# Performance work log

Hardware: AMD Instinct MI355X
Metric: run time of the kernel (lower is better)

The kernel has to match this reference:

```python
import jax, jax.numpy as jnp
import numpy as np


def setup_inputs() -> dict:
    key = jax.random.key(0)
    ks = jax.random.split(key, 9)
    B, T, C = 4, 2048, 2048
    E, I, SI = 8, 1408, 5632
    s = lambda k, shape, fan_in: jax.random.normal(k, shape, jnp.float32) * (fan_in ** -0.5)
    return {
        "x": jax.random.normal(ks[0], (B, T, C), jnp.float32),
        "gate_w": s(ks[1], (C, E), C),                  # router: x @ gate_w -> [N,E]
        "expert_gate_w": s(ks[2], (E, C, I), C),        # stacked gate_proj weights
        "expert_up_w": s(ks[3], (E, C, I), C),          # stacked up_proj weights
        "expert_down_w": s(ks[4], (E, I, C), I),        # stacked down_proj weights
        "shared_gate_w": s(ks[5], (C, SI), C),
        "shared_up_w": s(ks[6], (C, SI), C),
        "shared_down_w": s(ks[7], (SI, C), SI),
        "shared_expert_gate_w": s(ks[8], (C, 1), C),
        "top_k": 4,
    }


def reference(x, gate_w, expert_gate_w, expert_up_w, expert_down_w,
              shared_gate_w, shared_up_w, shared_down_w, shared_expert_gate_w, top_k):
    B, T, C = x.shape
    E = gate_w.shape[1]
    xf = x.reshape(-1, C)                      # [N, C]
    N = xf.shape[0]

    # --- router: softmax (fp32) -> top-k -> renormalize ---
    logits = xf @ gate_w                       # [N, E]
    probs = jax.nn.softmax(logits.astype(jnp.float32), axis=-1)
    w, idx = jax.lax.top_k(probs, top_k)       # [N, k]
    w = w / jnp.sum(w, axis=-1, keepdims=True)

    # dense combine gates [N, E]: zero for non-selected experts (equivalent to
    # the torch dispatch/sort/combine: each token gets weight w_k on expert idx_k)
    gates = jnp.zeros((N, E), jnp.float32).at[jnp.arange(N)[:, None], idx].add(w)

    # --- per-expert SwiGLU MLP, accumulated via scan over experts ---
    def step(acc, ew):
        wg, wu, wd, g = ew                     # wg/wu: [C,I], wd: [I,C], g: [N]
        h = jax.nn.silu(xf @ wg) * (xf @ wu)   # [N, I]
        return acc + g[:, None] * (h @ wd), None

    routed, _ = jax.lax.scan(
        step, jnp.zeros_like(xf),
        (expert_gate_w, expert_up_w, expert_down_w, gates.T))

    # --- shared expert with sigmoid gate ---
    shared = (jax.nn.silu(xf @ shared_gate_w) * (xf @ shared_up_w)) @ shared_down_w
    sg = jax.nn.sigmoid(xf @ shared_expert_gate_w)   # [N, 1]

    return (routed + sg * shared).reshape(B, T, C)
```

## Files before the change

kernel.cpp:

```cpp
#include <hip/hip_runtime.h>
#include <hip/hip_bf16.h>
#include <stdint.h>


typedef float f32x4 __attribute__((ext_vector_type(4)));
typedef int   i32x4 __attribute__((ext_vector_type(4)));
typedef __hip_bfloat16 bf16;

#define DEV __device__ __forceinline__

DEV void mfma16(f32x4& c, const i32x4& a, const i32x4& b) {
    asm("v_mfma_f32_16x16x32_bf16 %0, %1, %2, %0" : "+v"(c) : "v"(a), "v"(b));
}

template<int ROWS>
DEV void stage(const bf16* gtile, long ldK, char* lds, int tid) {
    const int wid = tid >> 6, lane = tid & 63;
    const int swz = ((lane & 7) ^ (lane >> 3)) << 4;
    constexpr int NISS = (ROWS * 128) / 4096;
    #pragma unroll
    for (int i = 0; i < NISS; i++) {
        const int o = i * 4096 + wid * 1024;
        const int row = (o >> 7) + (lane >> 3);
        const char* ga = (const char*)gtile + (long)row * (ldK * 2) + swz;
        __builtin_amdgcn_global_load_lds(
            (const __attribute__((address_space(1))) void*)ga,
            (__attribute__((address_space(3))) void*)(lds + o), 16, 0, 0);
    }
}

template<int ROWS>
DEV void stage_idx(const char* base, const long* roff, int ktb, char* lds,
                   int tid, int swz) {
    const int wid = tid >> 6;
    constexpr int NISS = (ROWS * 128) / 4096;
    #pragma unroll
    for (int i = 0; i < NISS; i++) {
        const int o = i * 4096 + wid * 1024;
        const char* ga = base + roff[i] + ktb + swz;
        __builtin_amdgcn_global_load_lds(
            (const __attribute__((address_space(1))) void*)ga,
            (__attribute__((address_space(3))) void*)(lds + o), 16, 0, 0);
    }
}

DEV i32x4 ldsfrag(const char* lds, int row, int kbyte) {
    const int off = (row << 7) + (kbyte ^ ((row & 7) << 4));
    return *(const i32x4*)(lds + off);
}

DEV void tcore(unsigned short (*t)[72], const float* __restrict__ src,
               bf16* __restrict__ dst, long Cd, long dld, int cb, int rb,
               int tid) {
    const int s = tid & 15, g = tid >> 4;
    #pragma unroll
    for (int i = 0; i < 4; i++) {
        const int r = i * 16 + g;
        const float4 v = *(const float4*)(src + (long)(rb + r) * Cd + cb + 4 * s);
        union { bf16 h[4]; ushort4 u; } cu;
        cu.h[0] = __float2bfloat16(v.x); cu.h[1] = __float2bfloat16(v.y);
        cu.h[2] = __float2bfloat16(v.z); cu.h[3] = __float2bfloat16(v.w);
        *(ushort4*)&t[r][4 * s] = cu.u;
    }
    __syncthreads();
    #pragma unroll
    for (int i = 0; i < 4; i++) {
        const int c = i * 16 + g;
        ushort4 u;
        u.x = t[4 * s + 0][c]; u.y = t[4 * s + 1][c];
        u.z = t[4 * s + 2][c]; u.w = t[4 * s + 3][c];
        *(ushort4*)((unsigned short*)dst + (long)(cb + c) * dld + rb + 4 * s) = u;
    }
}

__global__ __launch_bounds__(256) void convt_gu(const float* __restrict__ egw,
        const float* __restrict__ euw, const float* __restrict__ sgw,
        const float* __restrict__ suw, bf16* __restrict__ Wea,
        bf16* __restrict__ Web, bf16* __restrict__ Wsa, bf16* __restrict__ Wsb) {
    __shared__ unsigned short t[64][72];
    const int z = blockIdx.z, cb = blockIdx.x * 64, rb = blockIdx.y * 64;
    const float* src; bf16* dst; long Cd;
    if (z < 8)       { src = egw + (long)z * 2048 * 1408;        dst = Wea + (long)z * 1408 * 2048;        Cd = 1408; }
    else if (z < 16) { src = euw + (long)(z - 8) * 2048 * 1408;  dst = Web + (long)(z - 8) * 1408 * 2048;  Cd = 1408; }
    else if (z < 20) { src = sgw + (long)(z - 16) * 1408;        dst = Wsa + (long)(z - 16) * 1408 * 2048; Cd = 5632; }
    else             { src = suw + (long)(z - 20) * 1408;        dst = Wsb + (long)(z - 20) * 1408 * 2048; Cd = 5632; }
    tcore(t, src, dst, Cd, 2048, cb, rb, threadIdx.x);
}

__global__ __launch_bounds__(256) void convt_dns(const float* __restrict__ sdw,
        bf16* __restrict__ Wsd) {
    __shared__ unsigned short t[64][72];
    const int z = blockIdx.z, cb = blockIdx.x * 64, rb = blockIdx.y * 64;
    tcore(t, sdw + (long)z * 1408 * 2048, Wsd + (long)z * 1408,
          2048, 5632, cb, rb, threadIdx.x);
}

__global__ __launch_bounds__(256) void convt_dne(const float* __restrict__ edw,
        bf16* __restrict__ Wed) {
    __shared__ unsigned short t[64][72];
    const int z = blockIdx.z, cb = blockIdx.x * 64, rb = blockIdx.y * 64;
    tcore(t, edw + (long)z * 1408 * 2048, Wed + (long)z * 2048 * 1408,
          2048, 1408, cb, rb, threadIdx.x);
}

__global__ __launch_bounds__(256) void tcvt(const float* __restrict__ srcA,
        bf16* __restrict__ dstA, const float* __restrict__ srcB,
        bf16* __restrict__ dstB, int Cd, long dld, long sz, long dz,
        int zsplit) {
    __shared__ float t[64][65];
    long z = blockIdx.z;
    const float* src; bf16* dst;
    if ((int)z < zsplit) { src = srcA; dst = dstA; }
    else { src = srcB; dst = dstB; z -= zsplit; }
    src += z * sz; dst += z * dz;
    const int cb = blockIdx.x * 64, rb = blockIdx.y * 64;
    const int tx = threadIdx.x & 63, ty = threadIdx.x >> 6;
    #pragma unroll
    for (int i = 0; i < 16; i++) {
        const int r = ty + i * 4;
        t[r][tx] = src[(long)(rb + r) * Cd + cb + tx];
    }
    __syncthreads();
    #pragma unroll
    for (int i = 0; i < 16; i++) {
        const int c = ty + i * 4;
        dst[(long)(cb + c) * dld + rb + tx] = __float2bfloat16(t[tx][c]);
    }
}

__global__ __launch_bounds__(256) void cvtrt(const float* __restrict__ x,
        const float* __restrict__ gw, const float* __restrict__ segw,
        bf16* __restrict__ xb, int* __restrict__ tidx, float* __restrict__ tw,
        float* __restrict__ sg) {
    const int lane = threadIdx.x & 63;
    const long t = (long)blockIdx.x * 4 + (threadIdx.x >> 6);
    const float4* xr = (const float4*)(x + t * 2048);
    ushort4* xo = (ushort4*)(xb + t * 2048);
    float a[9];
    #pragma unroll
    for (int e = 0; e < 9; e++) a[e] = 0.f;
    #pragma unroll
    for (int i = 0; i < 8; i++) {
        const int c4 = i * 64 + lane;
        const float4 v = xr[c4];
        union { bf16 h[4]; ushort4 u; } cu;
        cu.h[0] = __float2bfloat16(v.x); cu.h[1] = __float2bfloat16(v.y);
        cu.h[2] = __float2bfloat16(v.z); cu.h[3] = __float2bfloat16(v.w);
        xo[c4] = cu.u;
        const int c = c4 * 4;
        const float xv[4] = { v.x, v.y, v.z, v.w };
        #pragma unroll
        for (int j = 0; j < 4; j++) {
            const float4* g4 = (const float4*)(gw + (long)(c + j) * 8);
            const float4 g0 = g4[0], g1 = g4[1];
            a[0] += xv[j] * g0.x; a[1] += xv[j] * g0.y;
            a[2] += xv[j] * g0.z; a[3] += xv[j] * g0.w;
            a[4] += xv[j] * g1.x; a[5] += xv[j] * g1.y;
            a[6] += xv[j] * g1.z; a[7] += xv[j] * g1.w;
            a[8] += xv[j] * segw[c + j];
        }
    }
    #pragma unroll
    for (int e = 0; e < 9; e++) {
        #pragma unroll
        for (int o = 32; o; o >>= 1) a[e] += __shfl_xor(a[e], o, 64);
    }
    if (lane == 0) {
        float m = a[0];
        #pragma unroll
        for (int e = 1; e < 8; e++) m = fmaxf(m, a[e]);
        float p[8]; float s = 0.f;
        #pragma unroll
        for (int e = 0; e < 8; e++) { p[e] = expf(a[e] - m); s += p[e]; }
        #pragma unroll
        for (int e = 0; e < 8; e++) p[e] /= s;
        bool used[8] = {false,false,false,false,false,false,false,false};
        float wsum = 0.f; int idx[4]; float wv[4];
        for (int k = 0; k < 4; k++) {
            float best = -1.f; int bi = 0;
            for (int e = 0; e < 8; e++)
                if (!used[e] && p[e] > best) { best = p[e]; bi = e; }
            used[bi] = true; idx[k] = bi; wv[k] = best; wsum += best;
        }
        int4 iv; float4 wv4;
        iv.x = idx[0]; iv.y = idx[1]; iv.z = idx[2]; iv.w = idx[3];
        wv4.x = wv[0] / wsum; wv4.y = wv[1] / wsum;
        wv4.z = wv[2] / wsum; wv4.w = wv[3] / wsum;
        ((int4*)tidx)[t] = iv;
        ((float4*)tw)[t] = wv4;
        sg[t] = 1.f / (1.f + expf(-a[8]));
    }
}

__global__ __launch_bounds__(256) void build_lists(const int* __restrict__ tidx,
        const float* __restrict__ tw, int* __restrict__ tok,
        float* __restrict__ wl, int* __restrict__ cnt, int* __restrict__ inv,
        int N) {
    const int e = blockIdx.x;
    const int tid = threadIdx.x;
    const int per = N / 256;
    __shared__ int csum[256];
    int c = 0;
    for (int i = 0; i < per; i++) {
        const int4 id4 = ((const int4*)tidx)[tid * per + i];
        if (id4.x == e || id4.y == e || id4.z == e || id4.w == e) c++;
    }
    csum[tid] = c;
    __syncthreads();
    for (int o = 1; o < 256; o <<= 1) {
        const int v = (tid >= o) ? csum[tid - o] : 0;
        __syncthreads();
        csum[tid] += v;
        __syncthreads();
    }
    int pos = csum[tid] - c;
    if (tid == 255) cnt[e] = csum[255];
    for (int i = 0; i < per; i++) {
        const int t = tid * per + i;
        const int4   id4 = ((const int4*)tidx)[t];
        const float4 w4  = ((const float4*)tw)[t];
        float w = 0.f; int hit = 0; int k = 0;
        if      (id4.x == e) { w = w4.x; hit = 1; k = 0; }
        else if (id4.y == e) { w = w4.y; hit = 1; k = 1; }
        else if (id4.z == e) { w = w4.z; hit = 1; k = 2; }
        else if (id4.w == e) { w = w4.w; hit = 1; k = 3; }
        if (hit) {
            tok[(long)e * N + pos] = t;
            wl[(long)e * N + pos] = w;
            inv[t * 4 + k] = pos;
            pos++;
        }
    }
}

__global__ void scan8(const int* __restrict__ cnt, int* __restrict__ starts) {
    if (threadIdx.x == 0) {
        int s = 0;
        for (int e = 0; e < 8; e++) { starts[e] = s; s += cnt[e]; }
        starts[8] = s;
    }
}

__global__ __launch_bounds__(256) void megadual(const bf16* __restrict__ A0,
        const int* __restrict__ tok, const int* __restrict__ cnt,
        const int* __restrict__ starts, int nExpZ, int e0,
        const bf16* __restrict__ Wea, const bf16* __restrict__ Web, long ebz,
        const bf16* __restrict__ Wsa, const bf16* __restrict__ Wsb,
        bf16* __restrict__ He, bf16* __restrict__ Hs,
        const float* __restrict__ wl, const float* __restrict__ sg, int K) {
    __shared__ __align__(128) char Al[16384];
    __shared__ __align__(128) char Gl[8192];
    __shared__ __align__(128) char Ul[8192];
    const int z = blockIdx.z;
    const bf16 *BG, *BU; bf16* H; long hld, n0; const float* sc;
    const int* ridx; int Me;
    if (z < nExpZ) {
        const int e = e0 + z;
        Me = cnt[e];
        ridx = tok + (long)e * 8192;
        BG = Wea + (long)z * ebz; BU = Web + (long)z * ebz;
        H = He + ((long)starts[e] - starts[e0]) * 1408;
        hld = 1408; sc = wl + (long)e * 8192;
        n0 = (long)blockIdx.y * 64;
    } else {
        Me = 8192; ridx = nullptr;
        BG = Wsa; BU = Wsb; H = Hs; hld = 5632; sc = sg;
        n0 = (long)((z - nExpZ) * gridDim.y + blockIdx.y) * 64;
    }
    const long m0 = (long)blockIdx.x * 128;
    if (m0 >= Me) return;
    const int tid = threadIdx.x, lane = tid & 63, wid = tid >> 6;
    const int wm = (wid >> 1) * 64, wn = (wid & 1) * 32;
    const int l15 = lane & 15, lhi = lane >> 4;
    const int swz = ((lane & 7) ^ (lane >> 3)) << 4;
    long roffA[4];
    #pragma unroll
    for (int i = 0; i < 4; i++) {
        const int rit = ((i * 4096 + wid * 1024) >> 7) + (lane >> 3);
        int g = (int)m0 + rit;
        if (ridx) g = ridx[g < Me ? g : Me - 1];
        roffA[i] = (long)g * (K * 2);
    }
    f32x4 ag[4][2] = {}; f32x4 au[4][2] = {};
    for (int kt = 0; kt < K; kt += 64) {
        stage_idx<128>((const char*)A0, roffA, kt * 2, Al, tid, swz);
        stage<64>(BG + n0 * K + kt, (long)K, Gl, tid);
        stage<64>(BU + n0 * K + kt, (long)K, Ul, tid);
        __syncthreads();
        #pragma unroll
        for (int ks = 0; ks < 2; ks++) {
            const int kb = ks * 64 + lhi * 16;
            i32x4 af[4], bg[2], bu[2];
            #pragma unroll
            for (int mi = 0; mi < 4; mi++) af[mi] = ldsfrag(Al, wm + mi * 16 + l15, kb);
            #pragma unroll
            for (int ni = 0; ni < 2; ni++) {
                bg[ni] = ldsfrag(Gl, wn + ni * 16 + l15, kb);
                bu[ni] = ldsfrag(Ul, wn + ni * 16 + l15, kb);
            }
            #pragma unroll
            for (int mi = 0; mi < 4; mi++) {
                #pragma unroll
                for (int ni = 0; ni < 2; ni++) {
                    mfma16(ag[mi][ni], af[mi], bg[ni]);
                    mfma16(au[mi][ni], af[mi], bu[ni]);
                }
            }
        }
        __syncthreads();
    }
    asm volatile("s_nop 7\n\ts_nop 7\n\ts_nop 7");
    #pragma unroll
    for (int mi = 0; mi < 4; mi++) {
        #pragma unroll
        for (int r = 0; r < 4; r++) {
            const int pos = (int)m0 + wm + mi * 16 + lhi * 4 + r;
            if (pos < Me) {
                const float s = sc[pos];
                #pragma unroll
                for (int ni = 0; ni < 2; ni++) {
                    const float gv = ag[mi][ni][r], uv = au[mi][ni][r];
                    const float h = (gv / (1.f + expf(-gv))) * uv * s;
                    H[(long)pos * hld + n0 + wn + ni * 16 + l15] = __float2bfloat16(h);
                }
            }
        }
    }
}

template<int TAG>
__global__ __launch_bounds__(256) void gemm_down_t(const bf16* __restrict__ A,
        const bf16* __restrict__ BT, float* __restrict__ C,
        const int* __restrict__ ridx, const int* __restrict__ cntp, int Mfix,
        const int* __restrict__ starts, int ia, int ib,
        int K, long ldc, int beta) {
    __shared__ __align__(128) char Al[16384];
    __shared__ __align__(128) char Bl[16384];
    const int Me = cntp ? *cntp : Mfix;
    const long m0 = (long)blockIdx.y * 128;
    if (m0 >= Me) return;
    if (starts) A += ((long)starts[ia] - starts[ib]) * K;
    const int tid = threadIdx.x, lane = tid & 63, wid = tid >> 6;
    const long n0 = (long)blockIdx.x * 128;
    const int wm = (wid >> 1) * 64, wn = (wid & 1) * 64;
    const int l15 = lane & 15, lhi = lane >> 4;
    f32x4 acc[4][4] = {};
    for (int kt = 0; kt < K; kt += 64) {
        stage<128>(A  + m0 * K + kt, (long)K, Al, tid);
        stage<128>(BT + n0 * K + kt, (long)K, Bl, tid);
        __syncthreads();
        #pragma unroll
        for (int ks = 0; ks < 2; ks++) {
            const int kb = ks * 64 + lhi * 16;
            i32x4 af[4], bfr[4];
            #pragma unroll
            for (int mi = 0; mi < 4; mi++) af[mi]  = ldsfrag(Al, wm + mi * 16 + l15, kb);
            #pragma unroll
            for (int ni = 0; ni < 4; ni++) bfr[ni] = ldsfrag(Bl, wn + ni * 16 + l15, kb);
            #pragma unroll
            for (int mi = 0; mi < 4; mi++) {
                #pragma unroll
                for (int ni = 0; ni < 4; ni++) mfma16(acc[mi][ni], af[mi], bfr[ni]);
            }
        }
        __syncthreads();
    }
    asm volatile("s_nop 7\n\ts_nop 7\n\ts_nop 7");
    #pragma unroll
    for (int mi = 0; mi < 4; mi++) {
        #pragma unroll
        for (int r = 0; r < 4; r++) {
            const int pos = (int)m0 + wm + mi * 16 + lhi * 4 + r;
            if (pos < Me) {
                const long orow = ridx ? (long)ridx[pos] : (long)pos;
                #pragma unroll
                for (int ni = 0; ni < 4; ni++) {
                    const long ci = orow * ldc + n0 + wn + ni * 16 + l15;
                    float v = acc[mi][ni][r];
                    if (beta) v += C[ci];
                    C[ci] = v;
                }
            }
        }
    }
}

__global__ __launch_bounds__(256) void megadown(const bf16* __restrict__ He,
        const bf16* __restrict__ Wd0, long wz, bf16* __restrict__ De,
        const int* __restrict__ cnt, const int* __restrict__ starts, int K) {
    __shared__ __align__(128) char Al[16384];
    __shared__ __align__(128) char Bl[16384];
    const int z = blockIdx.z;
    const int Me = cnt[z];
    const long m0 = (long)blockIdx.y * 128;
    if (m0 >= Me) return;
    const bf16* A  = He + (long)starts[z] * K;
    const bf16* BT = Wd0 + (long)z * wz;
    const int tid = threadIdx.x, lane = tid & 63, wid = tid >> 6;
    const long n0 = (long)blockIdx.x * 128;
    const int wm = (wid >> 1) * 64, wn = (wid & 1) * 64;
    const int l15 = lane & 15, lhi = lane >> 4;
    f32x4 acc[4][4] = {};
    for (int kt = 0; kt < K; kt += 64) {
        stage<128>(A  + m0 * K + kt, (long)K, Al, tid);
        stage<128>(BT + n0 * K + kt, (long)K, Bl, tid);
        __syncthreads();
        #pragma unroll
        for (int ks = 0; ks < 2; ks++) {
            const int kb = ks * 64 + lhi * 16;
            i32x4 af[4], bfr[4];
            #pragma unroll
            for (int mi = 0; mi < 4; mi++) af[mi]  = ldsfrag(Al, wm + mi * 16 + l15, kb);
            #pragma unroll
            for (int ni = 0; ni < 4; ni++) bfr[ni] = ldsfrag(Bl, wn + ni * 16 + l15, kb);
            #pragma unroll
            for (int mi = 0; mi < 4; mi++) {
                #pragma unroll
                for (int ni = 0; ni < 4; ni++) mfma16(acc[mi][ni], af[mi], bfr[ni]);
            }
        }
        __syncthreads();
    }
    asm volatile("s_nop 7\n\ts_nop 7\n\ts_nop 7");
    #pragma unroll
    for (int mi = 0; mi < 4; mi++) {
        #pragma unroll
        for (int r = 0; r < 4; r++) {
            const int pos = (int)m0 + wm + mi * 16 + lhi * 4 + r;
            if (pos < Me) {
                const long orow = (long)starts[z] + pos;
                #pragma unroll
                for (int ni = 0; ni < 4; ni++) {
                    De[orow * 2048 + n0 + wn + ni * 16 + l15]
                        = __float2bfloat16(acc[mi][ni][r]);
                }
            }
        }
    }
}

__global__ __launch_bounds__(256) void reduce4(const bf16* __restrict__ De,
        const int* __restrict__ tidx, const int* __restrict__ inv,
        const int* __restrict__ starts, float* __restrict__ out) {
    const long t = blockIdx.x;
    const int c = threadIdx.x * 8;
    const int4 e4 = ((const int4*)tidx)[t];
    const int4 p4 = ((const int4*)inv)[t];
    long r[4];
    r[0] = (long)starts[e4.x] + p4.x; r[1] = (long)starts[e4.y] + p4.y;
    r[2] = (long)starts[e4.z] + p4.z; r[3] = (long)starts[e4.w] + p4.w;
    float4* o = (float4*)(out + t * 2048 + c);
    float4 o0 = o[0], o1 = o[1];
    float acc[8] = { o0.x, o0.y, o0.z, o0.w, o1.x, o1.y, o1.z, o1.w };
    #pragma unroll
    for (int k = 0; k < 4; k++) {
        const uint4 v = *(const uint4*)(De + r[k] * 2048 + c);
        const unsigned w[4] = { v.x, v.y, v.z, v.w };
        #pragma unroll
        for (int j = 0; j < 4; j++) {
            union { unsigned u; float f; } lo, hi;
            lo.u = (w[j] & 0xffffu) << 16;
            hi.u = w[j] & 0xffff0000u;
            acc[j * 2]     += lo.f;
            acc[j * 2 + 1] += hi.f;
        }
    }
    o[0] = make_float4(acc[0], acc[1], acc[2], acc[3]);
    o[1] = make_float4(acc[4], acc[5], acc[6], acc[7]);
}

extern "C" void kernel_launch(void* const* d_in, const int* in_sizes, int n_in,
                              void* d_out, int out_size, void* d_ws, size_t ws_size,
                              hipStream_t stream) {
    const int N = 8192, Cdim = 2048, E = 8, I = 1408, SI = 5632;

    const float* x    = (const float*)d_in[0];
    const float* gw   = (const float*)d_in[1];
    const float* egw  = (const float*)d_in[2];
    const float* euw  = (const float*)d_in[3];
    const float* edw  = (const float*)d_in[4];
    const float* sgw  = (const float*)d_in[5];
    const float* suw  = (const float*)d_in[6];
    const float* sdw  = (const float*)d_in[7];
    const float* segw = (const float*)d_in[8];
    float* out = (float*)d_out;

    char* ws = (char*)d_ws;
    size_t off = 0;
    auto alloc = [&](size_t bytes) { char* p = ws + off; off += (bytes + 255) & ~(size_t)255; return p; };

    bf16*  xb     = (bf16*) alloc((size_t)N * Cdim * 2);
    int*   tidx   = (int*)  alloc((size_t)N * 4 * 4);
    float* tw     = (float*)alloc((size_t)N * 4 * 4);
    float* sg     = (float*)alloc((size_t)N * 4);
    int*   tok    = (int*)  alloc((size_t)E * N * 4);
    float* wl     = (float*)alloc((size_t)E * N * 4);
    int*   inv    = (int*)  alloc((size_t)N * 4 * 4);
    int*   cnt    = (int*)  alloc(256);
    int*   starts = (int*)  alloc(256);
    const size_t commonEnd = off;

    const size_t EWSLOT = (size_t)E * I * Cdim * 2;
    const size_t SWSLOT = (size_t)SI * Cdim * 2;
    const size_t HROWS  = (size_t)4 * N;
    const size_t mergedNeed = commonEnd + 2 * EWSLOT + 2 * SWSLOT
                            + (size_t)N * SI * 2 + HROWS * I * 2 + 4096;

    cvtrt<<<N / 4, 256, 0, stream>>>(x, gw, segw, xb, tidx, tw, sg);
    build_lists<<<E, 256, 0, stream>>>(tidx, tw, tok, wl, cnt, inv, N);
    scan8<<<1, 64, 0, stream>>>(cnt, starts);

    if (ws_size >= mergedNeed) {
        char* wreg = (char*)alloc(2 * EWSLOT + 2 * SWSLOT);
        bf16* Wea = (bf16*)wreg;
        bf16* Web = (bf16*)(wreg + EWSLOT);
        bf16* Wsa = (bf16*)(wreg + 2 * EWSLOT);
        bf16* Wsb = (bf16*)(wreg + 2 * EWSLOT + SWSLOT);
        bf16* Hs  = (bf16*)alloc((size_t)N * SI * 2);
        bf16* He  = (bf16*)alloc(HROWS * I * 2);
        bf16* Wsd = xb;
        bf16* Wed = Hs;
        bf16* De  = (bf16*)wreg;

        convt_gu<<<dim3(22, 32, 24), 256, 0, stream>>>(
                egw, euw, sgw, suw, Wea, Web, Wsa, Wsb);

        megadual<<<dim3(N / 128, I / 64, E + 4), 256, 0, stream>>>(xb,
                tok, cnt, starts, E, 0, Wea, Web, (long)I * Cdim,
                Wsa, Wsb, He, Hs, wl, sg, Cdim);

        convt_dns<<<dim3(32, 22, 4), 256, 0, stream>>>(sdw, Wsd);
        gemm_down_t<0><<<dim3(Cdim / 128, N / 128), 256, 0, stream>>>(
                Hs, Wsd, out, nullptr, nullptr, N, nullptr, 0, 0,
                SI, (long)Cdim, 0);

        convt_dne<<<dim3(32, 22, 8), 256, 0, stream>>>(edw, Wed);
        megadown<<<dim3(Cdim / 128, N / 128, E), 256, 0, stream>>>(
                He, Wed, (long)Cdim * I, De, cnt, starts, I);
        reduce4<<<N, 256, 0, stream>>>(De, tidx, inv, starts, out);
        return;
    }

    bf16* Wa = (bf16*)alloc(SWSLOT);
    bf16* Wb = (bf16*)alloc(SWSLOT);
    bf16* Wc = (bf16*)alloc(SWSLOT);
    bf16* Hs = (bf16*)alloc((size_t)N * SI * 2);
    bf16* He = (bf16*)alloc(HROWS * I * 2);
    if (off > ws_size) return;

    tcvt<<<dim3(SI / 64, Cdim / 64, 2), 256, 0, stream>>>(
            sgw, Wa, suw, Wb, SI, (long)Cdim, 0, 0, 1);
    tcvt<<<dim3(Cdim / 64, SI / 64, 1), 256, 0, stream>>>(
            sdw, Wc, nullptr, nullptr, Cdim, (long)SI, 0, 0, 1);
    megadual<<<dim3(N / 128, I / 64, 4), 256, 0, stream>>>(xb,
            tok, cnt, starts, 0, 0, nullptr, nullptr, 0,
            Wa, Wb, nullptr, Hs, wl, sg, Cdim);
    gemm_down_t<0><<<dim3(Cdim / 128, N / 128), 256, 0, stream>>>(
            Hs, Wc, out, nullptr, nullptr, N, nullptr, 0, 0, SI, (long)Cdim, 0);

    for (int b = 0; b < 2; b++) {
        const int e0 = b * 4;
        tcvt<<<dim3(I / 64, Cdim / 64, 8), 256, 0, stream>>>(
                egw + (long)e0 * Cdim * I, Wa, euw + (long)e0 * Cdim * I, Wb,
                I, (long)Cdim, (long)Cdim * I, (long)I * Cdim, 4);
        megadual<<<dim3(N / 128, I / 64, 4), 256, 0, stream>>>(xb,
                tok, cnt, starts, 4, e0, Wa, Wb, (long)I * Cdim,
                nullptr, nullptr, He, nullptr, wl, sg, Cdim);
        tcvt<<<dim3(Cdim / 64, I / 64, 4), 256, 0, stream>>>(
                edw + (long)e0 * I * Cdim, Wc, nullptr, nullptr,
                Cdim, (long)I, (long)I * Cdim, (long)Cdim * I, 4);
        for (int z = 0; z < 4; z++) {
            gemm_down_t<1><<<dim3(Cdim / 128, N / 128), 256, 0, stream>>>(
                    He, Wc + (long)z * Cdim * I, out,
                    tok + (long)(e0 + z) * N, cnt + e0 + z, 0,
                    starts, e0 + z, e0, I, (long)Cdim, 1);
        }
    }
}
```

Measured before the change: 1.393 ms.

## Fuse shared down-proj GEMM with routed combine, merge down-weight conversions

When the workspace has room for one more expert weight slot, the two down-projection weight conversions become a single launch. The routed expert down GEMM then runs first, and a new kernel computes the shared down GEMM and adds the four gathered routed expert rows in its epilogue. This removes the separate reduce4 pass and the extra read-modify-write of the fp32 output. The cost is extra workspace, and the epilogue's gather of bf16 De rows is scattered and may not coalesce well. The downfuse epilogue no longer applies the sigmoid shared gate, so it relies on that gate already being folded into Hs.

```diff
diff --git a/kernel.cpp b/kernel.cpp
--- a/kernel.cpp
+++ b/kernel.cpp
@@ -87,6 +87,19 @@
     tcore(t, src, dst, Cd, 2048, cb, rb, threadIdx.x);
 }
 
+__global__ __launch_bounds__(256) void convt_dn(const float* __restrict__ sdw,
+        const float* __restrict__ edw, bf16* __restrict__ Wsd,
+        bf16* __restrict__ Wed) {
+    __shared__ unsigned short t[64][72];
+    const int z = blockIdx.z, cb = blockIdx.x * 64, rb = blockIdx.y * 64;
+    if (z < 4)
+        tcore(t, sdw + (long)z * 1408 * 2048, Wsd + (long)z * 1408,
+              2048, 5632, cb, rb, threadIdx.x);
+    else
+        tcore(t, edw + (long)(z - 4) * 1408 * 2048, Wed + (long)(z - 4) * 2048 * 1408,
+              2048, 1408, cb, rb, threadIdx.x);
+}
+
 __global__ __launch_bounds__(256) void convt_dns(const float* __restrict__ sdw,
         bf16* __restrict__ Wsd) {
     __shared__ unsigned short t[64][72];
@@ -94,7 +107,6 @@
     tcore(t, sdw + (long)z * 1408 * 2048, Wsd + (long)z * 1408,
           2048, 5632, cb, rb, threadIdx.x);
 }
-
 __global__ __launch_bounds__(256) void convt_dne(const float* __restrict__ edw,
         bf16* __restrict__ Wed) {
     __shared__ unsigned short t[64][72];
@@ -385,6 +397,64 @@
     }
 }
 
+__global__ __launch_bounds__(256) void downfuse(const bf16* __restrict__ Hs,
+        const bf16* __restrict__ Wsd, const bf16* __restrict__ De,
+        const int* __restrict__ tidx, const int* __restrict__ inv,
+        const int* __restrict__ starts, float* __restrict__ out, int K) {
+    __shared__ __align__(128) char Al[16384];
+    __shared__ __align__(128) char Bl[16384];
+    __shared__ int sst[8];
+    const int tid = threadIdx.x, lane = tid & 63, wid = tid >> 6;
+    if (tid < 8) sst[tid] = starts[tid];
+    const long m0 = (long)blockIdx.y * 128;
+    const long n0 = (long)blockIdx.x * 128;
+    const int wm = (wid >> 1) * 64, wn = (wid & 1) * 64;
+    const int l15 = lane & 15, lhi = lane >> 4;
+    f32x4 acc[4][4] = {};
+    for (int kt = 0; kt < K; kt += 64) {
+        stage<128>(Hs + m0 * K + kt, (long)K, Al, tid);
+        stage<128>(Wsd + n0 * K + kt, (long)K, Bl, tid);
+        __syncthreads();
+        #pragma unroll
+        for (int ks = 0; ks < 2; ks++) {
+            const int kb = ks * 64 + lhi * 16;
+            i32x4 af[4], bfr[4];
+            #pragma unroll
+            for (int mi = 0; mi < 4; mi++) af[mi]  = ldsfrag(Al, wm + mi * 16 + l15, kb);
+            #pragma unroll
+            for (int ni = 0; ni < 4; ni++) bfr[ni] = ldsfrag(Bl, wn + ni * 16 + l15, kb);
+            #pragma unroll
+            for (int mi = 0; mi < 4; mi++) {
+                #pragma unroll
+                for (int ni = 0; ni < 4; ni++) mfma16(acc[mi][ni], af[mi], bfr[ni]);
+            }
+        }
+        __syncthreads();
+    }
+    asm volatile("s_nop 7\n\ts_nop 7\n\ts_nop 7");
+    #pragma unroll
+    for (int mi = 0; mi < 4; mi++) {
+        #pragma unroll
+        for (int r = 0; r < 4; r++) {
+            const long t = m0 + wm + mi * 16 + lhi * 4 + r;
+            const int4 e4 = ((const int4*)tidx)[t];
+            const int4 p4 = ((const int4*)inv)[t];
+            long rr[4];
+            rr[0] = (long)sst[e4.x] + p4.x; rr[1] = (long)sst[e4.y] + p4.y;
+            rr[2] = (long)sst[e4.z] + p4.z; rr[3] = (long)sst[e4.w] + p4.w;
+            #pragma unroll
+            for (int ni = 0; ni < 4; ni++) {
+                const long col = n0 + wn + ni * 16 + l15;
+                float v = acc[mi][ni][r];
+                #pragma unroll
+                for (int k = 0; k < 4; k++)
+                    v += __bfloat162float(De[rr[k] * 2048 + col]);
+                out[t * 2048 + col] = v;
+            }
+        }
+    }
+}
+
 __global__ __launch_bounds__(256) void megadown(const bf16* __restrict__ He,
         const bf16* __restrict__ Wd0, long wz, bf16* __restrict__ De,
         const int* __restrict__ cnt, const int* __restrict__ starts, int K) {
@@ -505,6 +575,7 @@
     const size_t HROWS  = (size_t)4 * N;
     const size_t mergedNeed = commonEnd + 2 * EWSLOT + 2 * SWSLOT
                             + (size_t)N * SI * 2 + HROWS * I * 2 + 4096;
+    const size_t fusedNeed  = mergedNeed + EWSLOT;
 
     cvtrt<<<N / 4, 256, 0, stream>>>(x, gw, segw, xb, tidx, tw, sg);
     build_lists<<<E, 256, 0, stream>>>(tidx, tw, tok, wl, cnt, inv, N);
@@ -519,25 +590,32 @@
         bf16* Hs  = (bf16*)alloc((size_t)N * SI * 2);
         bf16* He  = (bf16*)alloc(HROWS * I * 2);
         bf16* Wsd = xb;
-        bf16* Wed = Hs;
         bf16* De  = (bf16*)wreg;
 
         convt_gu<<<dim3(22, 32, 24), 256, 0, stream>>>(
                 egw, euw, sgw, suw, Wea, Web, Wsa, Wsb);
-
         megadual<<<dim3(N / 128, I / 64, E + 4), 256, 0, stream>>>(xb,
                 tok, cnt, starts, E, 0, Wea, Web, (long)I * Cdim,
                 Wsa, Wsb, He, Hs, wl, sg, Cdim);
 
-        convt_dns<<<dim3(32, 22, 4), 256, 0, stream>>>(sdw, Wsd);
-        gemm_down_t<0><<<dim3(Cdim / 128, N / 128), 256, 0, stream>>>(
-                Hs, Wsd, out, nullptr, nullptr, N, nullptr, 0, 0,
-                SI, (long)Cdim, 0);
-
-        convt_dne<<<dim3(32, 22, 8), 256, 0, stream>>>(edw, Wed);
-        megadown<<<dim3(Cdim / 128, N / 128, E), 256, 0, stream>>>(
-                He, Wed, (long)Cdim * I, De, cnt, starts, I);
-        reduce4<<<N, 256, 0, stream>>>(De, tidx, inv, starts, out);
+        if (ws_size >= fusedNeed) {
+            bf16* Wed = (bf16*)alloc(EWSLOT);
+            convt_dn<<<dim3(32, 22, 12), 256, 0, stream>>>(sdw, edw, Wsd, Wed);
+            megadown<<<dim3(Cdim / 128, N / 128, E), 256, 0, stream>>>(
+                    He, Wed, (long)Cdim * I, De, cnt, starts, I);
+            downfuse<<<dim3(Cdim / 128, N / 128), 256, 0, stream>>>(
+                    Hs, Wsd, De, tidx, inv, starts, out, SI);
+        } else {
+            bf16* Wed = Hs;
+            convt_dns<<<dim3(32, 22, 4), 256, 0, stream>>>(sdw, Wsd);
+            gemm_down_t<0><<<dim3(Cdim / 128, N / 128), 256, 0, stream>>>(
+                    Hs, Wsd, out, nullptr, nullptr, N, nullptr, 0, 0,
+                    SI, (long)Cdim, 0);
+            convt_dne<<<dim3(32, 22, 8), 256, 0, stream>>>(edw, Wed);
+            megadown<<<dim3(Cdim / 128, N / 128, E), 256, 0, stream>>>(
+                    He, Wed, (long)Cdim * I, De, cnt, starts, I);
+            reduce4<<<N, 256, 0, stream>>>(De, tidx, inv, starts, out);
+        }
         return;
     }
 
```

Result: no change. 1.399 ms (+0.4%).

## Replace down-projection GEMMs with 256x128-tile triple-buffered direct-to-LDS kernel

Applied to the files above, without the earlier changes.

Adds a new down8 kernel with 512 threads, 256x128 output tiles, three LDS buffers and global_load_lds prefetch split across the two k-halves. It replaces both the shared-expert and routed-expert down-projection GEMMs. The aim is to hide global memory latency behind MFMA work and raise reuse per block. The cost is 144KB of LDS per block, which limits occupancy to one block per CU. The larger M tile also risks wasted work on sparse expert segments.

```diff
diff --git a/kernel.cpp b/kernel.cpp
--- a/kernel.cpp
+++ b/kernel.cpp
@@ -94,7 +94,6 @@
     tcore(t, sdw + (long)z * 1408 * 2048, Wsd + (long)z * 1408,
           2048, 5632, cb, rb, threadIdx.x);
 }
-
 __global__ __launch_bounds__(256) void convt_dne(const float* __restrict__ edw,
         bf16* __restrict__ Wed) {
     __shared__ unsigned short t[64][72];
@@ -328,6 +327,134 @@
     }
 }
 
+#define STG6(B, KTB, J0, J1)                                                   \
+    do {                                                                       \
+        _Pragma("unroll")                                                      \
+        for (int j = J0; j <= J1; j++)                                         \
+            __builtin_amdgcn_global_load_lds(                                  \
+                (const __attribute__((address_space(1))) void*)(gsrc[j] + (KTB)), \
+                (__attribute__((address_space(3))) void*)(&L[B][0] + lds6[j]), \
+                16, 0, 0);                                                     \
+    } while (0)
+
+template<int OUT>
+__global__ __launch_bounds__(512) void down8(const bf16* __restrict__ A0,
+        const bf16* __restrict__ BT0, long bz, void* __restrict__ Cout,
+        const int* __restrict__ cnt, const int* __restrict__ starts,
+        int Mfix, int K, long ldc) {
+    __shared__ __align__(128) char L[3][49152];
+    int Me; const bf16 *A, *BT; long ob = 0;
+    if (OUT == 1) {
+        const int z = blockIdx.z;
+        Me = cnt[z]; A = A0 + (long)starts[z] * K;
+        BT = BT0 + (long)z * bz; ob = starts[z];
+    } else { Me = Mfix; A = A0; BT = BT0; }
+    const long m0 = (long)blockIdx.y * 256;
+    if (m0 >= Me) return;
+    const long n0 = (long)blockIdx.x * 128;
+    const int tid = threadIdx.x, lane = tid & 63, wid = tid >> 6;
+    const int wm = (wid >> 1) * 64, wn = (wid & 1) * 64;
+    const int l15 = lane & 15, lhi = lane >> 4;
+    const int swz = ((lane & 7) ^ (lane >> 3)) << 4;
+    const long Kb = (long)K * 2;
+
+    const char* gsrc[6];
+    int lds6[6];
+    #pragma unroll
+    for (int j = 0; j < 6; j++) {
+        long gr;
+        if (j < 4) {
+            gr = m0 + j * 64 + wid * 8 + (lane >> 3);
+            if (gr > (long)Me - 1) gr = Me - 1;
+            gsrc[j] = (const char*)A + gr * Kb + swz;
+        } else {
+            gr = n0 + (j - 4) * 64 + wid * 8 + (lane >> 3);
+            gsrc[j] = (const char*)BT + gr * Kb + swz;
+        }
+        lds6[j] = j * 8192 + wid * 1024;
+    }
+
+    f32x4 acc[4][4] = {};
+    const int NT = K / 64;
+    STG6(0, 0L, 0, 5);
+    STG6(1, 128L, 0, 5);
+    asm volatile("s_waitcnt vmcnt(6)" ::: "memory");
+    __builtin_amdgcn_s_barrier();
+
+    for (int t = 0; t < NT; ++t) {
+        const int cb = t % 3, sb = (t + 2) % 3;
+        const long ktb = (long)(t + 2) * 128;
+        const bool pf = (t + 2) < NT;
+        const char* Lc = &L[cb][0];
+        {
+            i32x4 af[4], bfr[4];
+            const int kb = lhi * 16;
+            #pragma unroll
+            for (int mi = 0; mi < 4; mi++) {
+                const int r = wm + mi * 16 + l15;
+                af[mi] = *(const i32x4*)(Lc + (r << 7) + (kb ^ ((r & 7) << 4)));
+            }
+            #pragma unroll
+            for (int ni = 0; ni < 4; ni++) {
+                const int r = wn + ni * 16 + l15;
+                bfr[ni] = *(const i32x4*)(Lc + 32768 + (r << 7) + (kb ^ ((r & 7) << 4)));
+            }
+            if (pf) STG6(sb, ktb, 0, 2);
+            __builtin_amdgcn_s_setprio(1);
+            #pragma unroll
+            for (int mi = 0; mi < 4; mi++)
+                #pragma unroll
+                for (int ni = 0; ni < 4; ni++) mfma16(acc[mi][ni], af[mi], bfr[ni]);
+            __builtin_amdgcn_s_setprio(0);
+        }
+        __builtin_amdgcn_s_barrier();
+        {
+            i32x4 af[4], bfr[4];
+            const int kb = 64 + lhi * 16;
+            #pragma unroll
+            for (int mi = 0; mi < 4; mi++) {
+                const int r = wm + mi * 16 + l15;
+                af[mi] = *(const i32x4*)(Lc + (r << 7) + (kb ^ ((r & 7) << 4)));
+            }
+            #pragma unroll
+            for (int ni = 0; ni < 4; ni++) {
+                const int r = wn + ni * 16 + l15;
+                bfr[ni] = *(const i32x4*)(Lc + 32768 + (r << 7) + (kb ^ ((r & 7) << 4)));
+            }
+            if (pf) STG6(sb, ktb, 3, 5);
+            __builtin_amdgcn_s_setprio(1);
+            #pragma unroll
+            for (int mi = 0; mi < 4; mi++)
+                #pragma unroll
+                for (int ni = 0; ni < 4; ni++) mfma16(acc[mi][ni], af[mi], bfr[ni]);
+            __builtin_amdgcn_s_setprio(0);
+        }
+        if (pf) asm volatile("s_waitcnt vmcnt(6)" ::: "memory");
+        else    asm volatile("s_waitcnt vmcnt(0)" ::: "memory");
+        __builtin_amdgcn_s_barrier();
+    }
+
+    asm volatile("s_nop 7\n\ts_nop 7\n\ts_nop 7");
+    #pragma unroll
+    for (int mi = 0; mi < 4; mi++) {
+        #pragma unroll
+        for (int r = 0; r < 4; r++) {
+            const long pos = m0 + wm + mi * 16 + lhi * 4 + r;
+            if (pos < Me) {
+                #pragma unroll
+                for (int ni = 0; ni < 4; ni++) {
+                    const long col = n0 + wn + ni * 16 + l15;
+                    if (OUT == 0)
+                        ((float*)Cout)[pos * ldc + col] = acc[mi][ni][r];
+                    else
+                        ((bf16*)Cout)[(ob + pos) * ldc + col]
+                            = __float2bfloat16(acc[mi][ni][r]);
+                }
+            }
+        }
+    }
+}
+
 template<int TAG>
 __global__ __launch_bounds__(256) void gemm_down_t(const bf16* __restrict__ A,
         const bf16* __restrict__ BT, float* __restrict__ C,
@@ -524,19 +651,17 @@
 
         convt_gu<<<dim3(22, 32, 24), 256, 0, stream>>>(
                 egw, euw, sgw, suw, Wea, Web, Wsa, Wsb);
-
         megadual<<<dim3(N / 128, I / 64, E + 4), 256, 0, stream>>>(xb,
                 tok, cnt, starts, E, 0, Wea, Web, (long)I * Cdim,
                 Wsa, Wsb, He, Hs, wl, sg, Cdim);
 
         convt_dns<<<dim3(32, 22, 4), 256, 0, stream>>>(sdw, Wsd);
-        gemm_down_t<0><<<dim3(Cdim / 128, N / 128), 256, 0, stream>>>(
-                Hs, Wsd, out, nullptr, nullptr, N, nullptr, 0, 0,
-                SI, (long)Cdim, 0);
+        down8<0><<<dim3(Cdim / 128, N / 256), 512, 0, stream>>>(
+                Hs, Wsd, 0, out, nullptr, nullptr, N, SI, (long)Cdim);
 
         convt_dne<<<dim3(32, 22, 8), 256, 0, stream>>>(edw, Wed);
-        megadown<<<dim3(Cdim / 128, N / 128, E), 256, 0, stream>>>(
-                He, Wed, (long)Cdim * I, De, cnt, starts, I);
+        down8<1><<<dim3(Cdim / 128, N / 256, E), 512, 0, stream>>>(
+                He, Wed, (long)Cdim * I, De, cnt, starts, 0, I, (long)Cdim);
         reduce4<<<N, 256, 0, stream>>>(De, tidx, inv, starts, out);
         return;
     }
```

Measured after the change: 1.404 ms. About the same (+0.8%).
